# Performance work log

Measured on AMD Instinct MI355X. Metric: run time of the kernel, lower is better.

## Reference

```python
import jax, jax.numpy as jnp
import numpy as np


def setup_inputs() -> dict:
    key = jax.random.key(0)
    k1, k2 = jax.random.split(key)
    B, G, P = 64, 4999, 50
    raw_gene_expr = jax.random.normal(k1, (B, G), dtype=jnp.float32)
    # binary pathway membership matrix, mimics torch.randint(0, 2, (P, G)).float()
    pathway_gene_matrix = (jax.random.uniform(k2, (P, G)) < 0.5).astype(jnp.float32)
    return {"raw_gene_expr": raw_gene_expr, "pathway_gene_matrix": pathway_gene_matrix}


def reference(raw_gene_expr, pathway_gene_matrix):
    """Vectorized ssGSEA enrichment (compute_pathway_activations0).

    raw_gene_expr:        [B, G] float
    pathway_gene_matrix:  [P, G] binary float
    returns:              [B, P] signed max-deviation enrichment scores
    """
    B, G = raw_gene_expr.shape
    P = pathway_gene_matrix.shape[0]

    # Sort genes per sample in descending expression order
    order = jnp.argsort(-raw_gene_expr, axis=1)                      # [B, G]
    sorted_expr = jnp.take_along_axis(raw_gene_expr, order, axis=1)  # [B, G]

    # hit[b, p, i] = 1 if gene at sorted position i belongs to pathway p
    hit = (pathway_gene_matrix[:, order] > 0)                        # [P, B, G]
    hit = jnp.transpose(hit, (1, 0, 2)).astype(raw_gene_expr.dtype)  # [B, P, G]

    size = jnp.sum(pathway_gene_matrix > 0, axis=1).astype(raw_gene_expr.dtype)  # [P]

    # Weighted hit increments: |expr|^0.25 over hits, normalized per (sample, pathway)
    w = (jnp.abs(sorted_expr) ** 0.25)[:, None, :] * hit             # [B, P, G]
    s = jnp.sum(w, axis=-1, keepdims=True)
    w = jnp.where(s > 0, w / jnp.where(s > 0, s, 1.0), w)

    cum_hit = jnp.cumsum(w, axis=-1)                                 # [B, P, G]
    denom = jnp.maximum(G - size, 1.0)[None, :, None]                # guard size==G
    cum_miss = jnp.cumsum((1.0 - hit) / denom, axis=-1)              # [B, P, G]

    running = cum_hit - cum_miss                                     # [B, P, G]
    pos = jnp.argmax(jnp.abs(running), axis=-1)                      # [B, P]
    # signed max deviation == running value at the argmax of |running|
    es = jnp.take_along_axis(running, pos[..., None], axis=-1)[..., 0]  # [B, P]
    es = jnp.where(size[None, :] > 0, es, 0.0)
    return es
```

## Files before the change

### kernel.cpp

```cpp
#include <hip/hip_runtime.h>
#include <math.h>

typedef unsigned long long ull;

constexpr int Bc = 64;
constexpr int Gc = 4999;
constexpr int Pc = 50;

constexpr int RUN   = 1024;
constexpr int NRUN  = 5;
constexpr int NPAD  = NRUN * RUN;
constexpr int LPW   = 79;
constexpr ull PADKEY = 0xFFFFFFFFFFFFFFFFull;

__device__ __forceinline__ ull shfl_xor64(ull v, int lm) {
    int lo = __shfl_xor((int)(unsigned)(v & 0xFFFFFFFFull), lm, 64);
    int hi = __shfl_xor((int)(unsigned)(v >> 32), lm, 64);
    return ((ull)(unsigned)hi << 32) | (unsigned)lo;
}

__global__ __launch_bounds__(256) void chunk_sort(
    const float* __restrict__ expr, const float* __restrict__ pathway,
    ull* __restrict__ runs, ull* __restrict__ pbits, int P, int G)
{
    __shared__ ull key[RUN];
    const int r = blockIdx.x, b = blockIdx.y, tid = threadIdx.x;
    const int base = tid * 4;
    const float* row = expr + (size_t)b * G;

    ull v[4];
#pragma unroll
    for (int o = 0; o < 4; ++o) {
        int i = r * RUN + base + o;
        if (i < G) {
            unsigned u = __float_as_uint(row[i]);
            unsigned m = (u >> 31) ? ~u : (u | 0x80000000u);
            v[o] = ((ull)(~m) << 32) | (unsigned)i;
        } else {
            v[o] = PADKEY;
        }
    }

    for (int kk = 2; kk <= RUN; kk <<= 1) {
        const int j0 = kk >> 1;
        if (j0 >= 256) {
#pragma unroll
            for (int o = 0; o < 4; ++o) key[base + o] = v[o];
            __syncthreads();
            for (int j = j0; j >= 256; j >>= 1) {
#pragma unroll
                for (int t = tid; t < RUN / 2; t += 256) {
                    int i  = ((t & ~(j - 1)) << 1) | (t & (j - 1));
                    int ix = i | j;
                    ull a = key[i], c = key[ix];
                    bool up = ((i & kk) == 0);
                    if ((a > c) == up) { key[i] = c; key[ix] = a; }
                }
                __syncthreads();
            }
#pragma unroll
            for (int o = 0; o < 4; ++o) v[o] = key[base + o];
        }
        int jstart = (j0 > 128) ? 128 : j0;
        for (int j = jstart; j >= 4; j >>= 1) {
            int lm = j >> 2;
            bool takeMin = (((tid & lm) == 0) == ((base & kk) == 0));
#pragma unroll
            for (int o = 0; o < 4; ++o) {
                ull c = shfl_xor64(v[o], lm);
                ull mn = (v[o] < c) ? v[o] : c;
                ull mx = (v[o] < c) ? c : v[o];
                v[o] = takeMin ? mn : mx;
            }
        }
#pragma unroll
        for (int j = 2; j >= 1; j >>= 1) {
            if (j < kk) {
#pragma unroll
                for (int o = 0; o < 4; ++o) {
                    if ((o & j) == 0) {
                        bool up = (((base + o) & kk) == 0);
                        ull a = v[o], c = v[o | j];
                        if ((a > c) == up) { v[o] = c; v[o | j] = a; }
                    }
                }
            }
        }
    }

    ull* dst = runs + ((size_t)b * NRUN + r) * RUN;
#pragma unroll
    for (int o = 0; o < 4; ++o) dst[base + o] = v[o];

    if (r == 0) {
        int g = b * 256 + tid;
        if (g < G) {
            ull m = 0;
#pragma unroll
            for (int p = 0; p < Pc; ++p)
                if (pathway[(size_t)p * G + g] > 0.0f) m |= (1ull << p);
            pbits[g] = m;
        }
    }
}

__global__ __launch_bounds__(1024) void rank_scatter(
    const ull* __restrict__ runs,
    float* __restrict__ wqout, unsigned short* __restrict__ sidxout, int G)
{
    __shared__ ull runsLDS[NPAD];
    const int rg = blockIdx.x, b = blockIdx.y, tid = threadIdx.x;

    const ull* rowruns = runs + (size_t)b * NPAD;
    for (int i = tid; i < NPAD; i += 1024) runsLDS[i] = rowruns[i];
    __syncthreads();

    const int e = rg * 1024 + tid;
    const ull keyv = runsLDS[e];
    if (keyv == PADKEY) return;

    const int run = e >> 10;
    int rank = e & 1023;
#pragma unroll
    for (int rr = 0; rr < NRUN; ++rr) {
        if (rr == run) continue;
        const ull* arr = &runsLDS[rr * RUN];
        int pos = 0;
#pragma unroll
        for (int s = RUN; s >= 1; s >>= 1) {
            int np = pos + s;
            if (np <= RUN && arr[np - 1] < keyv) pos = np;
        }
        rank += pos;
    }

    int idx = (int)(unsigned)(keyv & 0xFFFFFFFFu);
    unsigned m = ~((unsigned)(keyv >> 32));
    unsigned absbits = ((m >> 31) ? m : ~m) & 0x7FFFFFFFu;
    float av = __uint_as_float(absbits);
    wqout[(size_t)b * G + rank] = sqrtf(sqrtf(av));
    sidxout[(size_t)b * G + rank] = (unsigned short)idx;
}

__global__ __launch_bounds__(256) void es_kernel(
    const float* __restrict__ wq, const unsigned short* __restrict__ sidx,
    const ull* __restrict__ pbits, float* __restrict__ out, int B, int P, int G)
{
    __shared__ float    swq[Gc];
    __shared__ unsigned sm32[Gc];

    const int pg = blockIdx.x;
    const int b  = blockIdx.y;
    const int tid = threadIdx.x;
    const int pbeg = pg * 13;
    const int pend = (pbeg + 13 < P) ? (pbeg + 13) : P;

    for (int i = tid; i < G; i += 256) {
        swq[i]  = wq[(size_t)b * G + i];
        sm32[i] = (unsigned)(pbits[sidx[(size_t)b * G + i]] >> pbeg);
    }
    __syncthreads();

    const int lane = tid & 63;
    const int w = tid >> 6;
    const int p0 = pbeg + w * 4;
    if (p0 >= pend) return;
    const int sh4 = w * 4;

    const int start = lane * LPW;
    const int cnt = (start + LPW < G) ? LPW : (G - start);

    double sw[4] = {0.0, 0.0, 0.0, 0.0};
    int sh[4] = {0, 0, 0, 0};
    for (int k = 0; k < cnt; ++k) {
        int s = start + k;
        unsigned nib = (sm32[s] >> sh4) & 15u;
        double wv = (double)swq[s];
#pragma unroll
        for (int q = 0; q < 4; ++q) {
            if ((nib >> q) & 1u) { sw[q] += wv; sh[q]++; }
        }
    }
    double norm[4], inv_denom[4], running[4];
    int sht[4];
#pragma unroll
    for (int q = 0; q < 4; ++q) {
        double swt = sw[q];
        int shq = sh[q];
#pragma unroll
        for (int off = 1; off < 64; off <<= 1) {
            swt += __shfl_xor(swt, off, 64);
            shq += __shfl_xor(shq, off, 64);
        }
        sht[q] = shq;
        norm[q]      = (swt > 0.0) ? 1.0 / swt : 1.0;
        inv_denom[q] = 1.0 / fmax((double)(G - shq), 1.0);
        double csum = sw[q] * norm[q] - (double)(cnt - sh[q]) * inv_denom[q];
        double x = csum;
#pragma unroll
        for (int off = 1; off < 64; off <<= 1) {
            double vv = __shfl_up(x, off, 64);
            if (lane >= off) x += vv;
        }
        running[q] = x - csum;
    }

    double bestv[4] = {-1.0, -1.0, -1.0, -1.0};
    double bestr[4] = {0.0, 0.0, 0.0, 0.0};
    int besti[4] = {0x7FFFFFFF, 0x7FFFFFFF, 0x7FFFFFFF, 0x7FFFFFFF};
    for (int k = 0; k < cnt; ++k) {
        int s = start + k;
        unsigned nib = (sm32[s] >> sh4) & 15u;
        double wv = (double)swq[s];
#pragma unroll
        for (int q = 0; q < 4; ++q) {
            running[q] += ((nib >> q) & 1u) ? wv * norm[q] : -inv_denom[q];
            double a = fabs(running[q]);
            if (a > bestv[q]) { bestv[q] = a; bestr[q] = running[q]; besti[q] = s; }
        }
    }
#pragma unroll
    for (int q = 0; q < 4; ++q) {
#pragma unroll
        for (int off = 1; off < 64; off <<= 1) {
            double ov  = __shfl_xor(bestv[q], off, 64);
            double orr = __shfl_xor(bestr[q], off, 64);
            int    oi  = __shfl_xor(besti[q], off, 64);
            if (ov > bestv[q] || (ov == bestv[q] && oi < besti[q])) {
                bestv[q] = ov; bestr[q] = orr; besti[q] = oi;
            }
        }
    }

    if (lane == 0) {
#pragma unroll
        for (int q = 0; q < 4; ++q) {
            int p = p0 + q;
            if (p < pend)
                out[(size_t)b * P + p] = (sht[q] > 0) ? (float)bestr[q] : 0.0f;
        }
    }
}

extern "C" void kernel_launch(void* const* d_in, const int* in_sizes, int n_in,
                              void* d_out, int out_size, void* d_ws, size_t ws_size,
                              hipStream_t stream) {
    const float* expr    = (const float*)d_in[0];
    const float* pathway = (const float*)d_in[1];
    float* out = (float*)d_out;

    char* ws = (char*)d_ws;
    ull*            pbits = (ull*)ws;
    ull*            runs  = (ull*)(ws + 40960);
    float*          wqa   = (float*)(ws + 2662400);
    unsigned short* sidx  = (unsigned short*)(ws + 3942144);

    chunk_sort<<<dim3(NRUN, Bc), dim3(256), 0, stream>>>(
        expr, pathway, runs, pbits, Pc, Gc);
    rank_scatter<<<dim3(NRUN, Bc), dim3(1024), 0, stream>>>(runs, wqa, sidx, Gc);
    es_kernel<<<dim3(4, Bc), dim3(256), 0, stream>>>(
        wqa, sidx, pbits, out, Bc, Pc, Gc);
}
```

Measured before the change: 110.5 us.

## Split ES scan across two waves and pre-gather pathway bits in scatter

rank_scatter now writes the 64-bit pathway membership mask directly in sorted order, so es_kernel no longer does an indirect sidx→pbits gather. es_kernel doubles its threads to 512 and splits each pathway group's gene range across two waves of 41 elements per lane. Half sums and per-half argmax results are combined through shared memory. This halves the serial per-lane loop length at the cost of extra barriers and larger 8-byte writes in the scatter.

```diff
diff --git a/kernel.cpp b/kernel.cpp
--- a/kernel.cpp
+++ b/kernel.cpp
@@ -10,7 +10,8 @@
 constexpr int RUN   = 1024;
 constexpr int NRUN  = 5;
 constexpr int NPAD  = NRUN * RUN;
-constexpr int LPW   = 79;
+constexpr int LPW3  = 41;
+constexpr int HALF0 = 64 * LPW3;
 constexpr ull PADKEY = 0xFFFFFFFFFFFFFFFFull;
 
 __device__ __forceinline__ ull shfl_xor64(ull v, int lm) {
@@ -105,8 +106,8 @@
 }
 
 __global__ __launch_bounds__(1024) void rank_scatter(
-    const ull* __restrict__ runs,
-    float* __restrict__ wqout, unsigned short* __restrict__ sidxout, int G)
+    const ull* __restrict__ runs, const ull* __restrict__ pbits,
+    float* __restrict__ wqout, ull* __restrict__ pbout, int G)
 {
     __shared__ ull runsLDS[NPAD];
     const int rg = blockIdx.x, b = blockIdx.y, tid = threadIdx.x;
@@ -118,6 +119,9 @@
     const int e = rg * 1024 + tid;
     const ull keyv = runsLDS[e];
     if (keyv == PADKEY) return;
+
+    const int idx = (int)(unsigned)(keyv & 0xFFFFFFFFu);
+    const ull pb = pbits[idx];
 
     const int run = e >> 10;
     int rank = e & 1023;
@@ -134,20 +138,24 @@
         rank += pos;
     }
 
-    int idx = (int)(unsigned)(keyv & 0xFFFFFFFFu);
     unsigned m = ~((unsigned)(keyv >> 32));
     unsigned absbits = ((m >> 31) ? m : ~m) & 0x7FFFFFFFu;
     float av = __uint_as_float(absbits);
     wqout[(size_t)b * G + rank] = sqrtf(sqrtf(av));
-    sidxout[(size_t)b * G + rank] = (unsigned short)idx;
-}
-
-__global__ __launch_bounds__(256) void es_kernel(
-    const float* __restrict__ wq, const unsigned short* __restrict__ sidx,
-    const ull* __restrict__ pbits, float* __restrict__ out, int B, int P, int G)
+    pbout[(size_t)b * G + rank] = pb;
+}
+
+__global__ __launch_bounds__(512) void es_kernel(
+    const float* __restrict__ wq, const ull* __restrict__ pb64,
+    float* __restrict__ out, int B, int P, int G)
 {
     __shared__ float    swq[Gc];
     __shared__ unsigned sm32[Gc];
+    __shared__ double   cSW[4][2][4];
+    __shared__ int      cSH[4][2][4];
+    __shared__ double   cBV[4][2][4];
+    __shared__ double   cBR[4][2][4];
+    __shared__ int      cBI[4][2][4];
 
     const int pg = blockIdx.x;
     const int b  = blockIdx.y;
@@ -155,20 +163,22 @@
     const int pbeg = pg * 13;
     const int pend = (pbeg + 13 < P) ? (pbeg + 13) : P;
 
-    for (int i = tid; i < G; i += 256) {
+    for (int i = tid; i < G; i += 512) {
         swq[i]  = wq[(size_t)b * G + i];
-        sm32[i] = (unsigned)(pbits[sidx[(size_t)b * G + i]] >> pbeg);
+        sm32[i] = (unsigned)(pb64[(size_t)b * G + i] >> pbeg);
     }
     __syncthreads();
 
     const int lane = tid & 63;
-    const int w = tid >> 6;
-    const int p0 = pbeg + w * 4;
-    if (p0 >= pend) return;
-    const int sh4 = w * 4;
-
-    const int start = lane * LPW;
-    const int cnt = (start + LPW < G) ? LPW : (G - start);
+    const int w  = tid >> 6;
+    const int qg = w >> 1;
+    const int h  = w & 1;
+    const int sh4 = qg * 4;
+
+    const int lg = h * 64 + lane;
+    const int start = lg * LPW3;
+    int cnt = G - start;
+    cnt = (cnt < 0) ? 0 : ((cnt > LPW3) ? LPW3 : cnt);
 
     double sw[4] = {0.0, 0.0, 0.0, 0.0};
     int sh[4] = {0, 0, 0, 0};
@@ -181,20 +191,30 @@
             if ((nib >> q) & 1u) { sw[q] += wv; sh[q]++; }
         }
     }
+#pragma unroll
+    for (int q = 0; q < 4; ++q) {
+        double s_ = sw[q]; int c_ = sh[q];
+#pragma unroll
+        for (int off = 1; off < 64; off <<= 1) {
+            s_ += __shfl_xor(s_, off, 64);
+            c_ += __shfl_xor(c_, off, 64);
+        }
+        if (lane == 0) { cSW[qg][h][q] = s_; cSH[qg][h][q] = c_; }
+    }
+    __syncthreads();
+
     double norm[4], inv_denom[4], running[4];
-    int sht[4];
+    int shtot[4];
 #pragma unroll
     for (int q = 0; q < 4; ++q) {
-        double swt = sw[q];
-        int shq = sh[q];
-#pragma unroll
-        for (int off = 1; off < 64; off <<= 1) {
-            swt += __shfl_xor(swt, off, 64);
-            shq += __shfl_xor(shq, off, 64);
-        }
-        sht[q] = shq;
-        norm[q]      = (swt > 0.0) ? 1.0 / swt : 1.0;
-        inv_denom[q] = 1.0 / fmax((double)(G - shq), 1.0);
+        double s0 = cSW[qg][0][q], s1 = cSW[qg][1][q];
+        int    c0 = cSH[qg][0][q], c1 = cSH[qg][1][q];
+        double st = s0 + s1;
+        int    ct = c0 + c1;
+        shtot[q]     = ct;
+        norm[q]      = (st > 0.0) ? 1.0 / st : 1.0;
+        inv_denom[q] = 1.0 / fmax((double)(G - ct), 1.0);
+        double off1 = s0 * norm[q] - (double)(HALF0 - c0) * inv_denom[q];
         double csum = sw[q] * norm[q] - (double)(cnt - sh[q]) * inv_denom[q];
         double x = csum;
 #pragma unroll
@@ -202,7 +222,7 @@
             double vv = __shfl_up(x, off, 64);
             if (lane >= off) x += vv;
         }
-        running[q] = x - csum;
+        running[q] = x - csum + (h ? off1 : 0.0);
     }
 
     double bestv[4] = {-1.0, -1.0, -1.0, -1.0};
@@ -230,14 +250,18 @@
                 bestv[q] = ov; bestr[q] = orr; besti[q] = oi;
             }
         }
-    }
-
-    if (lane == 0) {
+        if (lane == 0) { cBV[qg][h][q] = bestv[q]; cBR[qg][h][q] = bestr[q]; cBI[qg][h][q] = besti[q]; }
+    }
+    __syncthreads();
+
+    if (h == 0 && lane == 0) {
 #pragma unroll
         for (int q = 0; q < 4; ++q) {
-            int p = p0 + q;
+            double v0 = cBV[qg][0][q], v1 = cBV[qg][1][q];
+            double r_ = (v1 > v0) ? cBR[qg][1][q] : cBR[qg][0][q];
+            int p = pbeg + sh4 + q;
             if (p < pend)
-                out[(size_t)b * P + p] = (sht[q] > 0) ? (float)bestr[q] : 0.0f;
+                out[(size_t)b * P + p] = (shtot[q] > 0) ? (float)r_ : 0.0f;
         }
     }
 }
@@ -250,14 +274,14 @@
     float* out = (float*)d_out;
 
     char* ws = (char*)d_ws;
-    ull*            pbits = (ull*)ws;
-    ull*            runs  = (ull*)(ws + 40960);
-    float*          wqa   = (float*)(ws + 2662400);
-    unsigned short* sidx  = (unsigned short*)(ws + 3942144);
+    ull*   pbits = (ull*)ws;
+    ull*   runs  = (ull*)(ws + 40960);
+    float* wqa   = (float*)(ws + 2662400);
+    ull*   pb64  = (ull*)(ws + 3942144);
 
     chunk_sort<<<dim3(NRUN, Bc), dim3(256), 0, stream>>>(
         expr, pathway, runs, pbits, Pc, Gc);
-    rank_scatter<<<dim3(NRUN, Bc), dim3(1024), 0, stream>>>(runs, wqa, sidx, Gc);
-    es_kernel<<<dim3(4, Bc), dim3(256), 0, stream>>>(
-        wqa, sidx, pbits, out, Bc, Pc, Gc);
-}
+    rank_scatter<<<dim3(NRUN, Bc), dim3(1024), 0, stream>>>(runs, pbits, wqa, pb64, Gc);
+    es_kernel<<<dim3(4, Bc), dim3(512), 0, stream>>>(
+        wqa, pb64, out, Bc, Pc, Gc);
+}
```

Result: faster. 103.7 us (-6.1%).
